# Optimization experiments

Hardware: AMD Instinct MI355X
Metric: run time of the kernel (lower is better)

Reference implementation:

```python
import jax, jax.numpy as jnp
import numpy as np

DIM = 1024; N_LAYERS = 4; N_HEADS = 16; HEAD_DIM = DIM // N_HEADS
HIDDEN = 2816; VOCAB = 256; EPS = 1e-5; THETA = 10000.0
B, S = 1, 2048


def _rmsnorm(x, w):
    xf = x.astype(jnp.float32)
    n = xf * jax.lax.rsqrt(jnp.mean(xf * xf, axis=-1, keepdims=True) + EPS)
    return n.astype(x.dtype) * w


def _rope(x, cos, sin):
    # x: [B,S,H,hd]; torch view_as_complex pairs consecutive elements (0,1),(2,3),...
    xr = x[..., 0::2].astype(jnp.float32)
    xi = x[..., 1::2].astype(jnp.float32)
    c = cos[None, :, None, :]
    s = sin[None, :, None, :]
    outr = xr * c - xi * s
    outi = xr * s + xi * c
    out = jnp.stack([outr, outi], axis=-1).reshape(x.shape)
    return out.astype(x.dtype)


def setup_inputs() -> dict:
    key = jax.random.key(0)
    ks = jax.random.split(key, 10)
    std = 0.02
    def w(k, shape):
        return jax.random.normal(k, shape, jnp.float32) * std
    return {
        "tokens": jax.random.randint(ks[0], (B, S), 0, VOCAB, dtype=jnp.int32),
        "tok_emb": w(ks[1], (VOCAB, DIM)),
        "wq": w(ks[2], (N_LAYERS, DIM, DIM)),
        "wk": w(ks[3], (N_LAYERS, DIM, DIM)),
        "wv": w(ks[4], (N_LAYERS, DIM, DIM)),
        "wo": w(ks[5], (N_LAYERS, DIM, DIM)),
        "w1": w(ks[6], (N_LAYERS, HIDDEN, DIM)),
        "w2": w(ks[7], (N_LAYERS, DIM, HIDDEN)),
        "w3": w(ks[8], (N_LAYERS, HIDDEN, DIM)),
        "attn_norm_w": jnp.ones((N_LAYERS, DIM), jnp.float32),
        "ffn_norm_w": jnp.ones((N_LAYERS, DIM), jnp.float32),
        "final_norm_w": jnp.ones((DIM,), jnp.float32),
        "out_w": w(ks[9], (VOCAB, DIM)),
    }


def reference(tokens, tok_emb, wq, wk, wv, wo, w1, w2, w3,
              attn_norm_w, ffn_norm_w, final_norm_w, out_w):
    seqlen = tokens.shape[1]
    # precompute_freqs_cis
    inv = 1.0 / (THETA ** (jnp.arange(0, HEAD_DIM, 2, dtype=jnp.float32) / HEAD_DIM))
    t = jnp.arange(seqlen, dtype=jnp.float32)
    freqs = jnp.outer(t, inv)          # [S, hd/2]
    cos, sin = jnp.cos(freqs), jnp.sin(freqs)
    scale = 1.0 / np.sqrt(HEAD_DIM)

    h = tok_emb[tokens]                # [B,S,D]

    def block(h, p):
        lwq, lwk, lwv, lwo, lw1, lw2, lw3, anw, fnw = p
        x = _rmsnorm(h, anw)
        q = (x @ lwq.T).reshape(B, seqlen, N_HEADS, HEAD_DIM)
        k = (x @ lwk.T).reshape(B, seqlen, N_HEADS, HEAD_DIM)
        v = (x @ lwv.T).reshape(B, seqlen, N_HEADS, HEAD_DIM)
        q = _rope(q, cos, sin)
        k = _rope(k, cos, sin)
        # non-causal full attention (eval mode: no diffusion mask, no dropout)
        scores = jnp.einsum('bqhd,bkhd->bhqk', q, k) * scale
        probs = jax.nn.softmax(scores, axis=-1)
        attn = jnp.einsum('bhqk,bkhd->bqhd', probs, v).reshape(B, seqlen, DIM)
        h = h + attn @ lwo.T
        x = _rmsnorm(h, fnw)
        ff = (jax.nn.silu(x @ lw1.T) * (x @ lw3.T)) @ lw2.T
        return h + ff, None

    h, _ = jax.lax.scan(block, h, (wq, wk, wv, wo, w1, w2, w3, attn_norm_w, ffn_norm_w))
    h = _rmsnorm(h, final_norm_w)
    # targets=None path: logits only for the last position
    return h[:, -1:, :] @ out_w.T      # [B,1,VOCAB]
```

## Files before the change

kernel.cpp:

```cpp
#include <hip/hip_runtime.h>
#include <stdint.h>

typedef __bf16 bf16;
typedef __bf16 bf16x4 __attribute__((ext_vector_type(4)));
typedef __bf16 bf16x8 __attribute__((ext_vector_type(8)));
typedef float f32x4 __attribute__((ext_vector_type(4)));
typedef float f32x16 __attribute__((ext_vector_type(16)));

#define SEQ 2048
#define DIM 1024
#define NHEAD 16
#define HDIM 64
#define HID 2816
#define NLAYER 4

__device__ __forceinline__ void gload_lds16(const void* g, void* l) {
  __builtin_amdgcn_global_load_lds(
      (const __attribute__((address_space(1))) void*)g,
      (__attribute__((address_space(3))) void*)l, 16, 0, 0);
}

template <int MODE, int BM, int BN>
__global__ __launch_bounds__(256) void gemm_bt(
    const bf16* __restrict__ A, const bf16* __restrict__ B,
    bf16* __restrict__ Cb, float* __restrict__ Cf, const float* R,
    int M, int N, int K)
{
  constexpr int MR = BM / 32;
  constexpr int NR = BN / 32;
  constexpr int LA = BM / 64;
  constexpr int LB = BN / 64;
  __shared__ bf16 As[2 * BM * 32];
  __shared__ bf16 Bs[2 * BN * 32];
  const int tid  = threadIdx.x;
  const int wv   = tid >> 6;
  const int lane = tid & 63;
  const int lo = lane & 15, hi = lane >> 4;
  const int row0 = blockIdx.y * BM;
  const int col0 = blockIdx.x * BN;
  const int wr = (wv >> 1) * (BM / 2);
  const int wc = (wv & 1) * (BN / 2);

  f32x4 acc[MR][NR];
  const f32x4 zero = {0.f, 0.f, 0.f, 0.f};
#pragma unroll
  for (int m = 0; m < MR; ++m)
#pragma unroll
    for (int n = 0; n < NR; ++n) acc[m][n] = zero;

  const bf16* ag = A + (size_t)(row0 + (tid >> 2)) * K + (tid & 3) * 8;
  const bf16* bg = B + (size_t)(col0 + (tid >> 2)) * K + (tid & 3) * 8;

  auto stage = [&](int buf, int k) {
#pragma unroll
    for (int i = 0; i < LA; ++i)
      gload_lds16(ag + k + (size_t)i*64*K, &As[buf*BM*32 + i*2048 + wv*512]);
#pragma unroll
    for (int i = 0; i < LB; ++i)
      gload_lds16(bg + k + (size_t)i*64*K, &Bs[buf*BN*32 + i*2048 + wv*512]);
  };
  auto compute = [&](int buf) {
    bf16x8 af[MR], bfv[NR];
#pragma unroll
    for (int m = 0; m < MR; ++m)
      af[m] = *(const bf16x8*)&As[buf*BM*32 + (wr + m*16 + lo)*32 + hi*8];
#pragma unroll
    for (int n = 0; n < NR; ++n)
      bfv[n] = *(const bf16x8*)&Bs[buf*BN*32 + (wc + n*16 + lo)*32 + hi*8];
#pragma unroll
    for (int m = 0; m < MR; ++m)
#pragma unroll
      for (int n = 0; n < NR; ++n)
        acc[m][n] = __builtin_amdgcn_mfma_f32_16x16x32_bf16(af[m], bfv[n], acc[m][n], 0, 0, 0);
  };

  stage(0, 0);
  __syncthreads();
  for (int k0 = 0; k0 < K; k0 += 64) {
    stage(1, k0 + 32);
    compute(0);
    __syncthreads();
    if (k0 + 64 < K) stage(0, k0 + 64);
    compute(1);
    __syncthreads();
  }

  if (MODE == 2) {
    const int hstride = N >> 1;
#pragma unroll
    for (int m = 0; m < MR; ++m)
#pragma unroll
      for (int p = 0; p < NR/2; ++p)
#pragma unroll
        for (int r = 0; r < 4; ++r) {
          const int row  = row0 + wr + m * 16 + hi * 4 + r;
          const int hcol = (col0 + wc)/2 + p * 16 + lo;
          float u = acc[m][2*p][r], g = acc[m][2*p+1][r];
          float y = u / (1.f + __expf(-u)) * g;
          Cb[(size_t)row * hstride + hcol] = (bf16)y;
        }
  } else {
#pragma unroll
    for (int m = 0; m < MR; ++m)
#pragma unroll
      for (int n = 0; n < NR; ++n)
#pragma unroll
        for (int r = 0; r < 4; ++r) {
          const int row = row0 + wr + m * 16 + hi * 4 + r;
          const int col = col0 + wc + n * 16 + lo;
          const size_t idx = (size_t)row * N + col;
          if (MODE == 0) Cb[idx] = (bf16)acc[m][n][r];
          else           Cf[idx] = R[idx] + acc[m][n][r];
        }
  }
}

__device__ __forceinline__ void softmax_pv(
    f32x16& s, float& m, float& lsum, f32x16& o0, f32x16& o1,
    const bf16x8 (&vf)[2][2], int h)
{
  float mx = s[0];
#pragma unroll
  for (int r = 1; r < 16; ++r) mx = fmaxf(mx, s[r]);
  mx = fmaxf(mx, __shfl_xor(mx, 32));
  if (!__all(mx <= m + 8.0f)) {
    float mnew = fmaxf(m, mx);
    float corr = __expf(m - mnew);
    m = mnew; lsum *= corr;
#pragma unroll
    for (int r = 0; r < 16; ++r) { o0[r] *= corr; o1[r] *= corr; }
  }
  float p[16]; float ps = 0.f;
#pragma unroll
  for (int r = 0; r < 16; ++r) { p[r] = __expf(s[r] - m); ps += p[r]; }
  ps += __shfl_xor(ps, 32);
  lsum += ps;

  unsigned int w[4][2];
#pragma unroll
  for (int g = 0; g < 4; ++g)
#pragma unroll
    for (int t2 = 0; t2 < 2; ++t2) {
      union { bf16 b[2]; unsigned int u; } pk;
      pk.b[0] = (bf16)p[g*4 + 2*t2];
      pk.b[1] = (bf16)p[g*4 + 2*t2 + 1];
      w[g][t2] = pk.u;
    }

#pragma unroll
  for (int c = 0; c < 2; ++c) {
    unsigned int keep0 = h ? w[2*c+1][0] : w[2*c][0];
    unsigned int keep1 = h ? w[2*c+1][1] : w[2*c][1];
    unsigned int send0 = h ? w[2*c][0]   : w[2*c+1][0];
    unsigned int send1 = h ? w[2*c][1]   : w[2*c+1][1];
    unsigned int r0 = __shfl_xor(send0, 32);
    unsigned int r1 = __shfl_xor(send1, 32);
    union { unsigned int u[4]; bf16x8 v; } pf;
    pf.u[0] = h ? r0 : keep0;
    pf.u[1] = h ? r1 : keep1;
    pf.u[2] = h ? keep0 : r0;
    pf.u[3] = h ? keep1 : r1;
    __builtin_amdgcn_s_setprio(1);
    o0 = __builtin_amdgcn_mfma_f32_32x32x16_bf16(vf[c][0], pf.v, o0, 0, 0, 0);
    o1 = __builtin_amdgcn_mfma_f32_32x32x16_bf16(vf[c][1], pf.v, o1, 0, 0, 0);
    __builtin_amdgcn_s_setprio(0);
  }
}

__device__ __forceinline__ void attn_tile64(
    const bf16* __restrict__ kb, const bf16* __restrict__ vb,
    const bf16x8 (&qfA)[4], const bf16x8 (&qfB)[4],
    bf16x8 (&kc)[4], bf16x8 (&kn)[4],
    f32x16& oA0, f32x16& oA1, f32x16& oB0, f32x16& oB1,
    float& mA, float& lA, float& mB, float& lB,
    int j0, int jn, int q5, int h)
{
  bf16x8 vf[2][2];
#pragma unroll
  for (int c = 0; c < 2; ++c)
#pragma unroll
    for (int dh = 0; dh < 2; ++dh)
      vf[c][dh] = *(const bf16x8*)&vb[(size_t)(dh*32 + q5)*2048 + j0 + c*16];
  {
    const bf16* kp = kb + (size_t)(jn + q5)*3072;
#pragma unroll
    for (int dc = 0; dc < 4; ++dc) kn[dc] = *(const bf16x8*)(kp + dc*16);
  }
  f32x16 sA, sB;
#pragma unroll
  for (int r = 0; r < 16; ++r) { sA[r] = 0.f; sB[r] = 0.f; }
  __builtin_amdgcn_s_setprio(1);
#pragma unroll
  for (int dc = 0; dc < 4; ++dc) {
    sA = __builtin_amdgcn_mfma_f32_32x32x16_bf16(kc[dc], qfA[dc], sA, 0, 0, 0);
    sB = __builtin_amdgcn_mfma_f32_32x32x16_bf16(kc[dc], qfB[dc], sB, 0, 0, 0);
  }
  __builtin_amdgcn_s_setprio(0);

  softmax_pv(sA, mA, lA, oA0, oA1, vf, h);
  softmax_pv(sB, mB, lB, oB0, oB1, vf, h);
}

__global__ __launch_bounds__(256, 2) void attn_kernel(const bf16* __restrict__ qkv,
    const bf16* __restrict__ vt, bf16* __restrict__ outb)
{
  __shared__ float Osh[4][32][65];
  __shared__ float msh[4][32];
  __shared__ float lsh[4][32];

  const int tid = threadIdx.x;
  const int wv = tid >> 6;
  const int lane = tid & 63;
  const int q5 = lane & 31, h = lane >> 5;
  const int hh = blockIdx.x;
  const int q0 = blockIdx.y * 64;

  bf16x8 qfA[4], qfB[4];
#pragma unroll
  for (int dc = 0; dc < 4; ++dc) {
    bf16x8 xa = *(const bf16x8*)&qkv[(size_t)(q0 + q5)*3072      + hh*64 + h*8 + dc*16];
    bf16x8 xb = *(const bf16x8*)&qkv[(size_t)(q0 + 32 + q5)*3072 + hh*64 + h*8 + dc*16];
#pragma unroll
    for (int j = 0; j < 8; ++j) {
      xa[j] = (bf16)(0.125f * (float)xa[j]);
      xb[j] = (bf16)(0.125f * (float)xb[j]);
    }
    qfA[dc] = xa; qfB[dc] = xb;
  }

  const bf16* kb = qkv + 1024 + hh*64 + h*8;
  const bf16* vb = vt + (size_t)hh*64*2048 + h*8;

  f32x16 oA0, oA1, oB0, oB1;
#pragma unroll
  for (int r = 0; r < 16; ++r) { oA0[r]=0.f; oA1[r]=0.f; oB0[r]=0.f; oB1[r]=0.f; }
  float mA = -1e30f, lA = 0.f, mB = -1e30f, lB = 0.f;

  bf16x8 ka[4], ka2[4];
  {
    const bf16* kp = kb + (size_t)(wv*32 + q5)*3072;
#pragma unroll
    for (int dc = 0; dc < 4; ++dc) ka[dc] = *(const bf16x8*)(kp + dc*16);
  }

  for (int t = 0; t < 16; t += 2) {
    attn_tile64(kb, vb, qfA, qfB, ka, ka2, oA0, oA1, oB0, oB1,
                mA, lA, mB, lB,
                (wv + 4*t)*32,     ((wv + 4*(t+1)) & 63)*32, q5, h);
    attn_tile64(kb, vb, qfA, qfB, ka2, ka, oA0, oA1, oB0, oB1,
                mA, lA, mB, lB,
                (wv + 4*(t+1))*32, ((wv + 4*(t+2)) & 63)*32, q5, h);
  }

  const int q = tid >> 3, d0 = (tid & 7) * 8;
#pragma unroll
  for (int pass = 0; pass < 2; ++pass) {
    const f32x16& p0 = pass ? oB0 : oA0;
    const f32x16& p1 = pass ? oB1 : oA1;
#pragma unroll
    for (int r = 0; r < 16; ++r) {
      const int dr = (r & 3) + 8*(r >> 2) + 4*h;
      Osh[wv][q5][dr]      = p0[r];
      Osh[wv][q5][32 + dr] = p1[r];
    }
    if (h == 0) {
      msh[wv][q5] = pass ? mB : mA;
      lsh[wv][q5] = pass ? lB : lA;
    }
    __syncthreads();
    {
      float mm = fmaxf(fmaxf(msh[0][q], msh[1][q]), fmaxf(msh[2][q], msh[3][q]));
      float e0 = __expf(msh[0][q] - mm), e1 = __expf(msh[1][q] - mm),
            e2 = __expf(msh[2][q] - mm), e3 = __expf(msh[3][q] - mm);
      float L = e0*lsh[0][q] + e1*lsh[1][q] + e2*lsh[2][q] + e3*lsh[3][q];
      float rinv = 1.0f / L;
      bf16x8 outv;
#pragma unroll
      for (int j = 0; j < 8; ++j) {
        float sum = e0*Osh[0][q][d0+j] + e1*Osh[1][q][d0+j]
                  + e2*Osh[2][q][d0+j] + e3*Osh[3][q][d0+j];
        outv[j] = (bf16)(sum * rinv);
      }
      *(bf16x8*)&outb[(size_t)(q0 + pass*32 + q)*DIM + hh*64 + d0] = outv;
    }
    __syncthreads();
  }
}

__global__ __launch_bounds__(256) void rope_init_kernel(float* __restrict__ ct, float* __restrict__ st) {
  int idx = blockIdx.x * 256 + threadIdx.x;
  if (idx >= SEQ * 32) return;
  int s = idx >> 5, i = idx & 31;
  float inv = powf(10000.0f, -(float)i / 32.0f);
  float f = (float)s * inv;
  ct[idx] = cosf(f);
  st[idx] = sinf(f);
}

__global__ __launch_bounds__(256) void cast_kernel(const float* __restrict__ src,
    bf16* __restrict__ dst, int perLayer, int dstStride, int dstOff, int L)
{
  int i = blockIdx.x * 256 + threadIdx.x;
  int e = i * 4;
  if (e >= perLayer * L) return;
  int l = e / perLayer;
  int o = e - l * perLayer;
  float4 v = *(const float4*)(src + e);
  bf16x4 b;
  b[0] = (bf16)v.x; b[1] = (bf16)v.y; b[2] = (bf16)v.z; b[3] = (bf16)v.w;
  *(bf16x4*)(dst + (size_t)l * dstStride + dstOff + o) = b;
}

__global__ __launch_bounds__(256) void cast_interleave_kernel(const float* __restrict__ src,
    bf16* __restrict__ dst, int isW3)
{
  const int PLh = HID * DIM;
  int i = blockIdx.x * 256 + threadIdx.x;
  int e = i * 4;
  if (e >= PLh * NLAYER) return;
  int l = e / PLh;
  int rem = e - l * PLh;
  int r = rem >> 10, c = rem & 1023;
  int dr = (r >> 4) * 32 + (isW3 ? 16 : 0) + (r & 15);
  float4 v = *(const float4*)(src + e);
  bf16x4 b;
  b[0] = (bf16)v.x; b[1] = (bf16)v.y; b[2] = (bf16)v.z; b[3] = (bf16)v.w;
  *(bf16x4*)(dst + (size_t)l * 2 * PLh + (size_t)dr * 1024 + c) = b;
}

__global__ __launch_bounds__(256) void embed_kernel(const int* __restrict__ tok,
    const float* __restrict__ emb, float* __restrict__ h)
{
  int s = blockIdx.x, t = threadIdx.x;
  int v = tok[s];
  ((float4*)(h + (size_t)s * DIM))[t] = ((const float4*)(emb + (size_t)v * DIM))[t];
}

__global__ __launch_bounds__(256) void rmsnorm_kernel(const float* __restrict__ h,
    const float* __restrict__ w, bf16* __restrict__ outb)
{
  int row = blockIdx.x, tid = threadIdx.x;
  float4 v = ((const float4*)(h + (size_t)row * DIM))[tid];
  float ss = v.x*v.x + v.y*v.y + v.z*v.z + v.w*v.w;
#pragma unroll
  for (int off = 1; off < 64; off <<= 1) ss += __shfl_xor(ss, off);
  __shared__ float red[4];
  if ((tid & 63) == 0) red[tid >> 6] = ss;
  __syncthreads();
  float tot = red[0] + red[1] + red[2] + red[3];
  float inv = rsqrtf(tot * (1.0f / DIM) + 1e-5f);
  float4 wv4 = ((const float4*)w)[tid];
  bf16x4 o;
  o[0] = (bf16)(v.x * inv * wv4.x);
  o[1] = (bf16)(v.y * inv * wv4.y);
  o[2] = (bf16)(v.z * inv * wv4.z);
  o[3] = (bf16)(v.w * inv * wv4.w);
  ((bf16x4*)(outb + (size_t)row * DIM))[tid] = o;
}

__global__ __launch_bounds__(256) void final_rms_kernel(const float* __restrict__ hrow,
    const float* __restrict__ w, float* __restrict__ fl)
{
  int tid = threadIdx.x;
  float4 v = ((const float4*)hrow)[tid];
  float ss = v.x*v.x + v.y*v.y + v.z*v.z + v.w*v.w;
#pragma unroll
  for (int off = 1; off < 64; off <<= 1) ss += __shfl_xor(ss, off);
  __shared__ float red[4];
  if ((tid & 63) == 0) red[tid >> 6] = ss;
  __syncthreads();
  float tot = red[0] + red[1] + red[2] + red[3];
  float inv = rsqrtf(tot * (1.0f / DIM) + 1e-5f);
  float4 wv4 = ((const float4*)w)[tid];
  float4 o;
  o.x = v.x * inv * wv4.x;
  o.y = v.y * inv * wv4.y;
  o.z = v.z * inv * wv4.z;
  o.w = v.w * inv * wv4.w;
  ((float4*)fl)[tid] = o;
}

__global__ __launch_bounds__(256) void rope_kernel(bf16* __restrict__ qkv,
    const float* __restrict__ ct, const float* __restrict__ st)
{
  int idx = blockIdx.x * 256 + threadIdx.x;
  if (idx >= SEQ * 128) return;
  int s = idx >> 7, rem = idx & 127;
  int h = rem >> 3, c8 = rem & 7;
  int d0 = c8 * 8, i0 = c8 * 4;
  float4 cv = *(const float4*)&ct[s*32 + i0];
  float4 sv = *(const float4*)&st[s*32 + i0];
  float c[4]  = {cv.x, cv.y, cv.z, cv.w};
  float sn[4] = {sv.x, sv.y, sv.z, sv.w};
  size_t base = (size_t)s * 3072 + h * 64 + d0;
#pragma unroll
  for (int part = 0; part < 2; ++part) {
    bf16x8 x = *(bf16x8*)&qkv[base + part * 1024];
    bf16x8 o;
#pragma unroll
    for (int p = 0; p < 4; ++p) {
      float xr = (float)x[2*p], xi = (float)x[2*p+1];
      o[2*p]   = (bf16)(xr * c[p] - xi * sn[p]);
      o[2*p+1] = (bf16)(xr * sn[p] + xi * c[p]);
    }
    *(bf16x8*)&qkv[base + part * 1024] = o;
  }
}

__global__ __launch_bounds__(256) void vtrans_kernel(const bf16* __restrict__ qkv,
    bf16* __restrict__ vt)
{
  __shared__ unsigned short T[64][66];
  const int tj = blockIdx.x & 31;
  const int td = blockIdx.x >> 5;
  const int t = threadIdx.x;
  {
    const int j = t >> 2, d0 = (t & 3) * 16;
    const bf16* src = qkv + (size_t)(tj*64 + j)*3072 + 2048 + td*64 + d0;
    bf16x8 a = *(const bf16x8*)src;
    bf16x8 b = *(const bf16x8*)(src + 8);
    union { bf16 v; unsigned short u; } cv;
#pragma unroll
    for (int i = 0; i < 8; ++i) {
      cv.v = a[i]; T[j][d0 + i] = cv.u;
      cv.v = b[i]; T[j][d0 + 8 + i] = cv.u;
    }
  }
  __syncthreads();
  {
    const int d = t >> 2, j0 = (t & 3) * 16;
    union { bf16x8 v; unsigned short u[8]; } oa, ob;
#pragma unroll
    for (int i = 0; i < 8; ++i) {
      oa.u[i] = T[j0 + i][d];
      ob.u[i] = T[j0 + 8 + i][d];
    }
    bf16* dst = vt + (size_t)(td*64 + d)*2048 + tj*64 + j0;
    *(bf16x8*)dst = oa.v;
    *(bf16x8*)(dst + 8) = ob.v;
  }
}

__global__ __launch_bounds__(64) void logits_kernel(const float* __restrict__ fl,
    const float* __restrict__ ow, float* __restrict__ outp)
{
  int v = blockIdx.x, lane = threadIdx.x;
  const float* row = ow + (size_t)v * DIM;
  float s = 0.f;
#pragma unroll
  for (int t = 0; t < 16; ++t) {
    int d = t * 64 + lane;
    s += fl[d] * row[d];
  }
#pragma unroll
  for (int off = 1; off < 64; off <<= 1) s += __shfl_xor(s, off);
  if (lane == 0) outp[v] = s;
}

extern "C" void kernel_launch(void* const* d_in, const int* in_sizes, int n_in,
                              void* d_out, int out_size, void* d_ws, size_t ws_size,
                              hipStream_t stream)
{
  const int*   tokens = (const int*)  d_in[0];
  const float* temb   = (const float*)d_in[1];
  const float* wq  = (const float*)d_in[2];
  const float* wk  = (const float*)d_in[3];
  const float* wvv = (const float*)d_in[4];
  const float* wo  = (const float*)d_in[5];
  const float* w1  = (const float*)d_in[6];
  const float* w2  = (const float*)d_in[7];
  const float* w3  = (const float*)d_in[8];
  const float* anw = (const float*)d_in[9];
  const float* fnw = (const float*)d_in[10];
  const float* finw= (const float*)d_in[11];
  const float* outw= (const float*)d_in[12];
  float* out = (float*)d_out;

  char* wsp = (char*)d_ws;
  size_t off = 0;
  auto take = [&](size_t bytes) -> void* {
    void* r = wsp + off;
    off += (bytes + 255) & ~(size_t)255;
    return r;
  };
  bf16* wqkv = (bf16*)take((size_t)NLAYER * 3072 * DIM * 2);
  bf16* wob  = (bf16*)take((size_t)NLAYER * DIM * DIM * 2);
  bf16* w13  = (bf16*)take((size_t)NLAYER * 2 * HID * DIM * 2);
  bf16* w2b  = (bf16*)take((size_t)NLAYER * DIM * HID * 2);
  float* h   = (float*)take((size_t)SEQ * DIM * 4);
  bf16* xn   = (bf16*)take((size_t)SEQ * DIM * 2);
  bf16* qkvb = (bf16*)take((size_t)SEQ * 3072 * 2);
  bf16* vtb  = (bf16*)take((size_t)DIM * SEQ * 2);
  bf16* attnb= (bf16*)take((size_t)SEQ * DIM * 2);
  bf16* hbb  = (bf16*)take((size_t)SEQ * HID * 2);
  float* ct  = (float*)take((size_t)SEQ * 32 * 4);
  float* st  = (float*)take((size_t)SEQ * 32 * 4);
  float* fl  = (float*)take((size_t)DIM * 4);

  rope_init_kernel<<<SEQ * 32 / 256, 256, 0, stream>>>(ct, st);

  const int PLd = DIM * DIM;
  const int PLh = HID * DIM;
  cast_kernel<<<PLd * NLAYER / 1024, 256, 0, stream>>>(wq,  wqkv, PLd, 3 * PLd, 0,       NLAYER);
  cast_kernel<<<PLd * NLAYER / 1024, 256, 0, stream>>>(wk,  wqkv, PLd, 3 * PLd, PLd,     NLAYER);
  cast_kernel<<<PLd * NLAYER / 1024, 256, 0, stream>>>(wvv, wqkv, PLd, 3 * PLd, 2 * PLd, NLAYER);
  cast_kernel<<<PLd * NLAYER / 1024, 256, 0, stream>>>(wo,  wob,  PLd, PLd,     0,       NLAYER);
  cast_interleave_kernel<<<PLh * NLAYER / 1024, 256, 0, stream>>>(w1, w13, 0);
  cast_interleave_kernel<<<PLh * NLAYER / 1024, 256, 0, stream>>>(w3, w13, 1);
  cast_kernel<<<PLh * NLAYER / 1024, 256, 0, stream>>>(w2,  w2b,  PLh, PLh,     0,       NLAYER);

  embed_kernel<<<SEQ, 256, 0, stream>>>(tokens, temb, h);

  for (int l = 0; l < NLAYER; ++l) {
    const bf16* lwqkv = wqkv + (size_t)l * 3 * PLd;
    const bf16* lwo   = wob  + (size_t)l * PLd;
    const bf16* lw13  = w13  + (size_t)l * 2 * PLh;
    const bf16* lw2   = w2b  + (size_t)l * PLh;

    rmsnorm_kernel<<<SEQ, 256, 0, stream>>>(h, anw + l * DIM, xn);
    gemm_bt<0,128,128><<<dim3(24, 16), 256, 0, stream>>>(xn, lwqkv, qkvb, nullptr, nullptr, SEQ, 3072, DIM);
    rope_kernel<<<SEQ * 128 / 256, 256, 0, stream>>>(qkvb, ct, st);
    vtrans_kernel<<<512, 256, 0, stream>>>(qkvb, vtb);
    attn_kernel<<<dim3(16, 32), 256, 0, stream>>>(qkvb, vtb, attnb);
    gemm_bt<1,64,64><<<dim3(16, 32), 256, 0, stream>>>(attnb, lwo, nullptr, h, h, SEQ, DIM, DIM);
    rmsnorm_kernel<<<SEQ, 256, 0, stream>>>(h, fnw + l * DIM, xn);
    gemm_bt<2,128,128><<<dim3(44, 16), 256, 0, stream>>>(xn, lw13, hbb, nullptr, nullptr, SEQ, 2 * HID, DIM);
    gemm_bt<1,64,64><<<dim3(16, 32), 256, 0, stream>>>(hbb, lw2, nullptr, h, h, SEQ, DIM, HID);
  }

  final_rms_kernel<<<1, 256, 0, stream>>>(h + (size_t)(SEQ - 1) * DIM, finw, fl);
  logits_kernel<<<256, 64, 0, stream>>>(fl, outw, out);
}
```

Before: 730.9 us.

## Split attention key range across 8 waves per block with 512 threads

The attention kernel now launches 512 threads (8 waves) per block instead of 256, and each wave processes half as many key tiles. The cross-wave merge grows to combine 8 partial softmax states, done in four passes over a smaller shared buffer that each write a 32-column half. The aim is more waves in flight per CU and a shorter serial loop per wave, hiding memory latency better. The cost is a larger merge with more barriers and narrower 4-byte output stores, plus the register pressure implied by launch bounds of (512,4).

After: 1.222 ms. +67.2%, slower.

```diff
diff --git a/kernel.cpp b/kernel.cpp
--- a/kernel.cpp
+++ b/kernel.cpp
@@ -201,12 +201,12 @@
   softmax_pv(sB, mB, lB, oB0, oB1, vf, h);
 }
 
-__global__ __launch_bounds__(256, 2) void attn_kernel(const bf16* __restrict__ qkv,
+__global__ __launch_bounds__(512, 4) void attn_kernel(const bf16* __restrict__ qkv,
     const bf16* __restrict__ vt, bf16* __restrict__ outb)
 {
-  __shared__ float Osh[4][32][65];
-  __shared__ float msh[4][32];
-  __shared__ float lsh[4][32];
+  __shared__ float Osh[8][32][33];
+  __shared__ float msh[8][32];
+  __shared__ float lsh[8][32];
 
   const int tid = threadIdx.x;
   const int wv = tid >> 6;
@@ -243,45 +243,48 @@
     for (int dc = 0; dc < 4; ++dc) ka[dc] = *(const bf16x8*)(kp + dc*16);
   }
 
-  for (int t = 0; t < 16; t += 2) {
+  for (int t = 0; t < 8; t += 2) {
     attn_tile64(kb, vb, qfA, qfB, ka, ka2, oA0, oA1, oB0, oB1,
                 mA, lA, mB, lB,
-                (wv + 4*t)*32,     ((wv + 4*(t+1)) & 63)*32, q5, h);
+                (wv + 8*t)*32,     ((wv + 8*(t+1)) & 63)*32, q5, h);
     attn_tile64(kb, vb, qfA, qfB, ka2, ka, oA0, oA1, oB0, oB1,
                 mA, lA, mB, lB,
-                (wv + 4*(t+1))*32, ((wv + 4*(t+2)) & 63)*32, q5, h);
-  }
-
-  const int q = tid >> 3, d0 = (tid & 7) * 8;
-#pragma unroll
-  for (int pass = 0; pass < 2; ++pass) {
-    const f32x16& p0 = pass ? oB0 : oA0;
-    const f32x16& p1 = pass ? oB1 : oA1;
+                (wv + 8*(t+1))*32, ((wv + 8*(t+2)) & 63)*32, q5, h);
+  }
+
+  const int q = tid >> 4;
+  const int dpair = tid & 15;
+#pragma unroll
+  for (int pass = 0; pass < 4; ++pass) {
+    const int qt = pass >> 1;
+    const int dh = pass & 1;
+    const f32x16& po = (pass == 0) ? oA0 : (pass == 1) ? oA1
+                     : (pass == 2) ? oB0 : oB1;
 #pragma unroll
     for (int r = 0; r < 16; ++r) {
       const int dr = (r & 3) + 8*(r >> 2) + 4*h;
-      Osh[wv][q5][dr]      = p0[r];
-      Osh[wv][q5][32 + dr] = p1[r];
-    }
-    if (h == 0) {
-      msh[wv][q5] = pass ? mB : mA;
-      lsh[wv][q5] = pass ? lB : lA;
-    }
+      Osh[wv][q5][dr] = po[r];
+    }
+    if (h == 0) { msh[wv][q5] = qt ? mB : mA; lsh[wv][q5] = qt ? lB : lA; }
     __syncthreads();
     {
-      float mm = fmaxf(fmaxf(msh[0][q], msh[1][q]), fmaxf(msh[2][q], msh[3][q]));
-      float e0 = __expf(msh[0][q] - mm), e1 = __expf(msh[1][q] - mm),
-            e2 = __expf(msh[2][q] - mm), e3 = __expf(msh[3][q] - mm);
-      float L = e0*lsh[0][q] + e1*lsh[1][q] + e2*lsh[2][q] + e3*lsh[3][q];
+      float mm = msh[0][q];
+#pragma unroll
+      for (int w = 1; w < 8; ++w) mm = fmaxf(mm, msh[w][q]);
+      float e[8], L = 0.f;
+#pragma unroll
+      for (int w = 0; w < 8; ++w) { e[w] = __expf(msh[w][q] - mm); L += e[w]*lsh[w][q]; }
       float rinv = 1.0f / L;
-      bf16x8 outv;
-#pragma unroll
-      for (int j = 0; j < 8; ++j) {
-        float sum = e0*Osh[0][q][d0+j] + e1*Osh[1][q][d0+j]
-                  + e2*Osh[2][q][d0+j] + e3*Osh[3][q][d0+j];
-        outv[j] = (bf16)(sum * rinv);
+      float s0 = 0.f, s1 = 0.f;
+#pragma unroll
+      for (int w = 0; w < 8; ++w) {
+        s0 += e[w] * Osh[w][q][2*dpair];
+        s1 += e[w] * Osh[w][q][2*dpair + 1];
       }
-      *(bf16x8*)&outb[(size_t)(q0 + pass*32 + q)*DIM + hh*64 + d0] = outv;
+      union { bf16 b[2]; unsigned int u; } ov;
+      ov.b[0] = (bf16)(s0 * rinv);
+      ov.b[1] = (bf16)(s1 * rinv);
+      *(unsigned int*)&outb[(size_t)(q0 + qt*32 + q)*DIM + hh*64 + dh*32 + 2*dpair] = ov.u;
     }
     __syncthreads();
   }
@@ -521,7 +524,7 @@
     gemm_bt<0,128,128><<<dim3(24, 16), 256, 0, stream>>>(xn, lwqkv, qkvb, nullptr, nullptr, SEQ, 3072, DIM);
     rope_kernel<<<SEQ * 128 / 256, 256, 0, stream>>>(qkvb, ct, st);
     vtrans_kernel<<<512, 256, 0, stream>>>(qkvb, vtb);
-    attn_kernel<<<dim3(16, 32), 256, 0, stream>>>(qkvb, vtb, attnb);
+    attn_kernel<<<dim3(16, 32), 512, 0, stream>>>(qkvb, vtb, attnb);
     gemm_bt<1,64,64><<<dim3(16, 32), 256, 0, stream>>>(attnb, lwo, nullptr, h, h, SEQ, DIM, DIM);
     rmsnorm_kernel<<<SEQ, 256, 0, stream>>>(h, fnw + l * DIM, xn);
     gemm_bt<2,128,128><<<dim3(44, 16), 256, 0, stream>>>(xn, lw13, hbb, nullptr, nullptr, SEQ, 2 * HID, DIM);
```
